# Kernel optimization log

Measured on AMD Instinct MI355X. Metric: run time of the kernel, lower is better.

Reference implementation:

```python
import jax, jax.numpy as jnp
import numpy as np

DIM = 512; NHEAD = 8; DHEAD = 64; INNER = NHEAD * DHEAD
CTX = 1024; NOCT = int(np.ceil(np.log2(CTX))) + 1  # 11
B = 8; SEQ = 256; MEM = 768


def positional_encoding(ctx, num_oct):
    # matches Attention.positional_encoding on coords=arange(ctx).view(ctx,1),
    # start_octave = 1 - num_oct
    coords = jnp.arange(ctx, dtype=jnp.float32)[:, None, None]        # (ctx,1,1)
    octaves = jnp.arange(1 - num_oct, 1, dtype=jnp.float32)           # (num_oct,)
    mult = (2.0 ** octaves) * np.pi
    scaled = (coords * mult).reshape(ctx, num_oct)                    # (ctx, num_oct)
    return jnp.concatenate([jnp.sin(scaled), jnp.cos(scaled)], axis=-1)  # (ctx, 2*num_oct)


def get_shifts(mem, seq, ctx):
    coords = jnp.arange(mem + seq - 1, -1, -1) - (seq - 1)            # (mem+seq,)
    shifts = coords[None, :] + jnp.arange(seq)[:, None]               # (seq, mem+seq)
    oob = (shifts < 0) | (shifts > ctx - 1)
    bias = jnp.where(oob, -jnp.inf, 0.0).astype(jnp.float32)
    return jnp.clip(shifts, 0, ctx - 1), bias


def setup_inputs() -> dict:
    key = jax.random.key(0)
    ks = jax.random.split(key, 8)
    s = 0.02
    return {
        "x": jax.random.normal(ks[0], (B, SEQ, DIM), jnp.float32),
        "memory": jax.random.normal(ks[1], (B, MEM, DIM), jnp.float32),
        "W_qkv": jax.random.normal(ks[2], (DIM, 3 * INNER), jnp.float32) * s,
        "W_rel": jax.random.normal(ks[3], (2 * NOCT, INNER), jnp.float32) * s,
        "W_out": jax.random.normal(ks[4], (INNER, DIM), jnp.float32) * s,
        "b_out": jnp.zeros((DIM,), jnp.float32),
        "u_emb": jax.random.normal(ks[5], (DHEAD,), jnp.float32),
        "v_emb": jax.random.normal(ks[6], (DHEAD,), jnp.float32),
    }


def reference(x, memory, W_qkv, W_rel, W_out, b_out, u_emb, v_emb):
    b, seq, _ = x.shape
    mem = memory.shape[1]
    total = mem + seq
    scale = DHEAD ** -0.5

    shifts, bias = get_shifts(mem, seq, CTX)                          # (seq,total) each
    R = positional_encoding(CTX, NOCT)                                # (CTX, 2*NOCT)
    kr = (R @ W_rel)[shifts].reshape(seq, total, NHEAD, DHEAD)        # n m h d

    qkv = jnp.concatenate([memory, x], axis=1) @ W_qkv                # (b,total,3*INNER)
    q, k, v = jnp.split(qkv, 3, axis=-1)

    def heads(t):
        return t.reshape(b, total, NHEAD, DHEAD).transpose(0, 2, 1, 3)  # b h m d

    q = heads(q)[:, :, mem:]                                          # b h n d (queries only over x)
    k = heads(k)
    v = heads(v)

    term_a = jnp.einsum('bhnd,bhmd->bhnm', q, k)
    term_b = jnp.einsum('bhnd,nmhd->bhnm', q, kr)
    term_c = jnp.einsum('d,bhmd->bhm', u_emb, k)[:, :, None, :]        # broadcast over n
    term_d = jnp.einsum('d,nmhd->hnm', v_emb, kr)[None]                # broadcast over b

    dots = (term_a + term_b + term_c + term_d) * scale + bias          # banded -inf mask
    attn = jax.nn.softmax(dots, axis=-1)                               # dropout p=0 -> identity
    out = jnp.einsum('bhnm,bhmd->bnhd', attn, v).reshape(b, seq, INNER)
    return out @ W_out + b_out
```

## Files before the change

kernel.cpp:

```cpp
#include <hip/hip_runtime.h>
#include <hip/hip_bf16.h>
#include <math.h>

typedef unsigned short u16;
typedef unsigned int u32;
typedef __attribute__((ext_vector_type(8))) short short8;
typedef __attribute__((ext_vector_type(4))) float floatx4;

constexpr int kB     = 8;
constexpr int kSEQ   = 256;
constexpr int kMEM   = 768;
constexpr int kTOTAL = 1024;

__device__ __forceinline__ float bf2f(u16 u) {
  return __uint_as_float(((u32)u) << 16);
}
__device__ __forceinline__ u16 f2bf(float f) {
  __hip_bfloat16 h = __float2bfloat16(f);
  return *reinterpret_cast<u16*>(&h);
}
__device__ __forceinline__ void gload_lds16(const u16* g, u16* l) {
  __builtin_amdgcn_global_load_lds(
      (__attribute__((address_space(1))) const unsigned int*)g,
      (__attribute__((address_space(3))) unsigned int*)l, 16, 0, 0);
}

__device__ __forceinline__ void wtconv_body(
    const float* __restrict__ W, u16* __restrict__ Wt, int K, int N,
    int n0, int k0, int tid, float (*tile)[65])
{
  int r = tid >> 4, c4 = (tid & 15) * 4;
#pragma unroll
  for (int v = 0; v < 4; v++) {
    float4 w4 = *(const float4*)(W + (size_t)(k0 + v * 16 + r) * N + n0 + c4);
    tile[v * 16 + r][c4 + 0] = w4.x;
    tile[v * 16 + r][c4 + 1] = w4.y;
    tile[v * 16 + r][c4 + 2] = w4.z;
    tile[v * 16 + r][c4 + 3] = w4.w;
  }
  __syncthreads();
#pragma unroll
  for (int v = 0; v < 4; v++) {
    int rn = v * 16 + r;
    ushort4 o;
    o.x = f2bf(tile[c4 + 0][rn]);
    o.y = f2bf(tile[c4 + 1][rn]);
    o.z = f2bf(tile[c4 + 2][rn]);
    o.w = f2bf(tile[c4 + 3][rn]);
    *(ushort4*)(Wt + (size_t)(n0 + rn) * K + k0 + c4) = o;
  }
}

__global__ __launch_bounds__(256) void prep_kernel(
    const float* __restrict__ x, const float* __restrict__ memf,
    const float* __restrict__ W_qkv, const float* __restrict__ W_out,
    const float* __restrict__ W_rel, const float* __restrict__ v_emb,
    u16* __restrict__ Xb, u16* __restrict__ WqkvT, u16* __restrict__ WoutT,
    u16* __restrict__ Rrel_bf, float* __restrict__ vR)
{
  __shared__ float tile[64][65];
  __shared__ float pe[22];
  __shared__ float prod[512];
  int bid = blockIdx.x;
  int t = threadIdx.x;
  if (bid < 1024) {
    int s = bid;
    if (t < 22) {
      int o = (t < 11) ? t : (t - 11);
      float mult = ldexpf(3.14159265358979323846f, o - 10);
      float ang = (float)s * mult;
      pe[t] = (t < 11) ? sinf(ang) : cosf(ang);
    }
    __syncthreads();
#pragma unroll
    for (int c = 0; c < 2; c++) {
      int j = t + c * 256;
      float acc = 0.f;
#pragma unroll
      for (int o = 0; o < 22; ++o) acc += pe[o] * W_rel[o * 512 + j];
      Rrel_bf[(size_t)s * 512 + j] = f2bf(acc);
      prod[j] = acc * v_emb[j & 63];
    }
    __syncthreads();
    if (t < 8) {
      float a = 0.f;
#pragma unroll 8
      for (int d = 0; d < 64; d++) a += prod[t * 64 + d];
      vR[t * 1024 + s] = a * 0.125f;
    }
  } else if (bid < 3072) {
    int idx = (bid - 1024) * 256 + t;
    int row = idx >> 6, c8 = idx & 63;
    int b = row >> 10, pos = row & 1023;
    const float* src = (pos < kMEM)
        ? memf + (size_t)(b * kMEM + pos) * 512
        : x    + (size_t)(b * kSEQ + pos - kMEM) * 512;
    const float4* s4 = (const float4*)(src + c8 * 8);
    float4 a = s4[0], bb = s4[1];
    u16 tmp[8] = {f2bf(a.x),  f2bf(a.y),  f2bf(a.z),  f2bf(a.w),
                  f2bf(bb.x), f2bf(bb.y), f2bf(bb.z), f2bf(bb.w)};
    *(uint4*)(Xb + (size_t)row * 512 + c8 * 8) = *(uint4*)tmp;
  } else if (bid < 3264) {
    int r = bid - 3072;
    wtconv_body(W_qkv, WqkvT, 512, 1536, (r % 24) * 64, (r / 24) * 64, t, tile);
  } else {
    int r = bid - 3264;
    wtconv_body(W_out, WoutT, 512, 512, (r % 8) * 64, (r / 8) * 64, t, tile);
  }
}

__global__ __launch_bounds__(256) void gemm_bf16(
    const u16* __restrict__ A, const u16* __restrict__ Bt,
    int lda, int ldb, int ksteps,
    u16* __restrict__ Cbf, int ldc, int qscale)
{
  __shared__ u16 As[128 * 64];
  __shared__ u16 Bs[128 * 64];
  int tid = threadIdx.x;
  int id = blockIdx.y * gridDim.x + blockIdx.x;
  int gy = gridDim.y;
  int bm = (id % gy) * 128, bn = (id / gy) * 128;
  int ln = tid & 15, quad = (tid >> 4) & 3, w = tid >> 6;
  int moff = (w >> 1) * 64, noff = (w & 1) * 64;
  int l7 = ln & 7;
  floatx4 acc[4][4];
#pragma unroll
  for (int mi = 0; mi < 4; mi++)
#pragma unroll
    for (int ni = 0; ni < 4; ni++) acc[mi][ni] = (floatx4){0.f, 0.f, 0.f, 0.f};

  int srow[4], sgch[4];
#pragma unroll
  for (int v = 0; v < 4; v++) {
    int f = v * 256 + tid;
    srow[v] = f >> 3;
    sgch[v] = (f & 7) ^ ((f >> 3) & 7);
  }

  for (int ks = 0; ks < ksteps; ks++) {
    int k0 = ks * 64;
#pragma unroll
    for (int v = 0; v < 4; v++) {
      gload_lds16(A + (size_t)(bm + srow[v]) * lda + k0 + sgch[v] * 8,
                  &As[(v * 256 + tid) * 8]);
      gload_lds16(Bt + (size_t)(bn + srow[v]) * ldb + k0 + sgch[v] * 8,
                  &Bs[(v * 256 + tid) * 8]);
    }
    __syncthreads();
#pragma unroll
    for (int kb = 0; kb < 2; kb++) {
      short8 af[4], bfr[4];
#pragma unroll
      for (int mi = 0; mi < 4; mi++) {
        int row = moff + mi * 16 + ln;
        af[mi] = *(const short8*)&As[row * 64 + (((quad + 4 * kb) ^ l7) << 3)];
      }
#pragma unroll
      for (int ni = 0; ni < 4; ni++) {
        int row = noff + ni * 16 + ln;
        bfr[ni] = *(const short8*)&Bs[row * 64 + (((quad + 4 * kb) ^ l7) << 3)];
      }
#pragma unroll
      for (int mi = 0; mi < 4; mi++)
#pragma unroll
        for (int ni = 0; ni < 4; ni++)
          acc[mi][ni] = __builtin_amdgcn_mfma_f32_16x16x32_bf16(
              af[mi], bfr[ni], acc[mi][ni], 0, 0, 0);
    }
    __syncthreads();
  }

  int r0 = bm + moff + quad * 4;
#pragma unroll
  for (int ni = 0; ni < 4; ni++) {
    int col = bn + noff + ni * 16 + ln;
    float scale = (qscale && col < 512) ? 0.125f : 1.f;
#pragma unroll
    for (int mi = 0; mi < 4; mi++) {
#pragma unroll
      for (int r = 0; r < 4; r++) {
        int row = r0 + mi * 16 + r;
        Cbf[(size_t)row * ldc + col] = f2bf(acc[mi][ni][r] * scale);
      }
    }
  }
}

__global__ __launch_bounds__(256) void gemm_bf16_64(
    const u16* __restrict__ A, const u16* __restrict__ Bt,
    int lda, int ldb, int ksteps,
    float* __restrict__ Cf, int ldc, const float* __restrict__ bias)
{
  __shared__ u16 As[64 * 64];
  __shared__ u16 Bs[64 * 64];
  int tid = threadIdx.x;
  int id = blockIdx.y * gridDim.x + blockIdx.x;
  int gy = gridDim.y;
  int bm = (id % gy) * 64, bn = (id / gy) * 64;
  int ln = tid & 15, quad = (tid >> 4) & 3, w = tid >> 6;
  int moff = (w >> 1) * 32, noff = (w & 1) * 32;
  int l7 = ln & 7;
  floatx4 acc[2][2];
#pragma unroll
  for (int mi = 0; mi < 2; mi++)
#pragma unroll
    for (int ni = 0; ni < 2; ni++) acc[mi][ni] = (floatx4){0.f, 0.f, 0.f, 0.f};

  int srow[2], sgch[2];
#pragma unroll
  for (int v = 0; v < 2; v++) {
    int f = v * 256 + tid;
    srow[v] = f >> 3;
    sgch[v] = (f & 7) ^ ((f >> 3) & 7);
  }

  for (int ks = 0; ks < ksteps; ks++) {
    int k0 = ks * 64;
#pragma unroll
    for (int v = 0; v < 2; v++) {
      gload_lds16(A + (size_t)(bm + srow[v]) * lda + k0 + sgch[v] * 8,
                  &As[(v * 256 + tid) * 8]);
      gload_lds16(Bt + (size_t)(bn + srow[v]) * ldb + k0 + sgch[v] * 8,
                  &Bs[(v * 256 + tid) * 8]);
    }
    __syncthreads();
#pragma unroll
    for (int kb = 0; kb < 2; kb++) {
      short8 af[2], bfr[2];
#pragma unroll
      for (int mi = 0; mi < 2; mi++) {
        int row = moff + mi * 16 + ln;
        af[mi] = *(const short8*)&As[row * 64 + (((quad + 4 * kb) ^ l7) << 3)];
      }
#pragma unroll
      for (int ni = 0; ni < 2; ni++) {
        int row = noff + ni * 16 + ln;
        bfr[ni] = *(const short8*)&Bs[row * 64 + (((quad + 4 * kb) ^ l7) << 3)];
      }
#pragma unroll
      for (int mi = 0; mi < 2; mi++)
#pragma unroll
        for (int ni = 0; ni < 2; ni++)
          acc[mi][ni] = __builtin_amdgcn_mfma_f32_16x16x32_bf16(
              af[mi], bfr[ni], acc[mi][ni], 0, 0, 0);
    }
    __syncthreads();
  }

  int r0 = bm + moff + quad * 4;
#pragma unroll
  for (int ni = 0; ni < 2; ni++) {
    int col = bn + noff + ni * 16 + ln;
    float cv = bias[col];
#pragma unroll
    for (int mi = 0; mi < 2; mi++) {
#pragma unroll
      for (int r = 0; r < 4; r++) {
        int row = r0 + mi * 16 + r;
        Cf[(size_t)row * ldc + col] = acc[mi][ni][r] + cv;
      }
    }
  }
}

__global__ __launch_bounds__(256) void attn_mfma(
    const u16* __restrict__ qkv_bf, const u16* __restrict__ Rrel_bf,
    const float* __restrict__ vR, const float* __restrict__ u_emb,
    u16* __restrict__ Opart, float* __restrict__ lbuf)
{
  constexpr int LD  = 72;
  constexpr int TLD = 84;
  __shared__ u16 Vt[2][64 * LD];
  __shared__ u16 Ps[64 * LD];
  __shared__ u16 Tl[4 * 16 * TLD];

  int nt = blockIdx.x >> 3, p = blockIdx.x & 7;
  int h = blockIdx.y, b = blockIdx.z;
  int n0 = nt * 64, bh = b * 8 + h;
  int tid = threadIdx.x;
  int w = tid >> 6, lane = tid & 63;
  int l15 = lane & 15, quad = lane >> 4, q8 = quad * 8;

  int sr0 = tid >> 3, sc8 = tid & 7;
  int sr1 = (256 + tid) >> 3;
  int vg0 = ((sr0 >> 3) ^ sc8) * 8 + (sr0 & 7);
  int vg1 = ((sr1 >> 3) ^ sc8) * 8 + (sr1 & 7);

  const u16* qrow = qkv_bf + (size_t)(b * kTOTAL + kMEM + n0 + 16 * w + l15) * 1536 + h * 64;
  short8 qf0 = *(const short8*)(qrow + q8);
  short8 qf1 = *(const short8*)(qrow + 32 + q8);

  short8 uf0, uf1;
  {
    u16 t0[8], t1[8];
#pragma unroll
    for (int j = 0; j < 8; j++) {
      t0[j] = f2bf(0.125f * u_emb[q8 + j]);
      t1[j] = f2bf(0.125f * u_emb[32 + q8 + j]);
    }
    uf0 = *(short8*)t0;
    uf1 = *(short8*)t1;
  }

  const u16* kpart = qkv_bf + (size_t)(b * kTOTAL) * 1536 + 512 + h * 64;
  const float* vRh = vR + h * 1024;
  u16* Tw = Tl + w * 16 * TLD;

  int ntiles = 13 + nt;
  int mtA = p, mtB = p + 8;
  bool hasB = (mtB < ntiles);
  bool lastB = (mtB == ntiles - 1);

  {
    const u16* va = kpart + (size_t)mtA * 64 * 1536 + 512;
    const u16* vb = kpart + (size_t)mtB * 64 * 1536 + 512;
    uint4 a0 = *(const uint4*)(va + (size_t)sr0 * 1536 + sc8 * 8);
    uint4 a1 = *(const uint4*)(va + (size_t)sr1 * 1536 + sc8 * 8);
    uint4 b0 = *(const uint4*)(vb + (size_t)sr0 * 1536 + sc8 * 8);
    uint4 b1 = *(const uint4*)(vb + (size_t)sr1 * 1536 + sc8 * 8);
    const u16* pa0v = (const u16*)&a0;
    const u16* pa1v = (const u16*)&a1;
    const u16* pb0v = (const u16*)&b0;
    const u16* pb1v = (const u16*)&b1;
#pragma unroll
    for (int i = 0; i < 8; i++) {
      Vt[0][(sc8 * 8 + i) * LD + vg0] = pa0v[i];
      Vt[0][(sc8 * 8 + i) * LD + vg1] = pa1v[i];
      Vt[1][(sc8 * 8 + i) * LD + vg0] = pb0v[i];
      Vt[1][(sc8 * 8 + i) * LD + vg1] = pb1v[i];
    }
  }
  __syncthreads();

  floatx4 o_acc[4];
  float l_i[4];
#pragma unroll
  for (int r = 0; r < 4; r++) l_i[r] = 0.f;
#pragma unroll
  for (int nd = 0; nd < 4; nd++) o_acc[nd] = (floatx4){0.f, 0.f, 0.f, 0.f};

  int s_base_w = kMEM + n0 + 16 * w;

  auto tile_body = [&](int mt, bool lastt, const u16* VtX) {
    int m0 = mt * 64;
    const u16* kbase = kpart + (size_t)m0 * 1536;
    int sb = s_base_w - m0;

    short8 kb0[4], kb1[4];
#pragma unroll
    for (int ni = 0; ni < 4; ni++) {
      const u16* kr = kbase + (size_t)(16 * ni + l15) * 1536;
      kb0[ni] = *(const short8*)(kr + q8);
      kb1[ni] = *(const short8*)(kr + 32 + q8);
    }
    short8 rb0[5], rb1[5];
    float vRc[5];
#pragma unroll
    for (int ct = 0; ct < 5; ct++) {
      int s = sb - 63 + 16 * ct + l15;
      s = min(max(s, 0), 1023);
      const u16* rr = Rrel_bf + (size_t)s * 512 + h * 64;
      rb0[ct] = *(const short8*)(rr + q8);
      rb1[ct] = *(const short8*)(rr + 32 + q8);
      vRc[ct] = vRh[s];
    }

    floatx4 uku[4];
#pragma unroll
    for (int ni = 0; ni < 4; ni++) {
      floatx4 ua = (floatx4){0.f, 0.f, 0.f, 0.f};
      ua = __builtin_amdgcn_mfma_f32_16x16x32_bf16(uf0, kb0[ni], ua, 0, 0, 0);
      ua = __builtin_amdgcn_mfma_f32_16x16x32_bf16(uf1, kb1[ni], ua, 0, 0, 0);
      uku[ni] = ua;
    }

#pragma unroll
    for (int ct = 0; ct < 5; ct++) {
      floatx4 t = (floatx4){0.f, 0.f, 0.f, 0.f};
      t = __builtin_amdgcn_mfma_f32_16x16x32_bf16(qf0, rb0[ct], t, 0, 0, 0);
      t = __builtin_amdgcn_mfma_f32_16x16x32_bf16(qf1, rb1[ct], t, 0, 0, 0);
#pragma unroll
      for (int r = 0; r < 4; r++)
        Tw[(4 * quad + r) * TLD + 16 * ct + l15] = f2bf(t[r] + vRc[ct]);
    }

    floatx4 s_acc[4];
#pragma unroll
    for (int ni = 0; ni < 4; ni++) {
      floatx4 sa = (floatx4){0.f, 0.f, 0.f, 0.f};
      sa = __builtin_amdgcn_mfma_f32_16x16x32_bf16(qf0, kb0[ni], sa, 0, 0, 0);
      sa = __builtin_amdgcn_mfma_f32_16x16x32_bf16(qf1, kb1[ni], sa, 0, 0, 0);
      s_acc[ni] = sa;
    }

#pragma unroll
    for (int r = 0; r < 4; r++) {
      int il = 4 * quad + r;
      float ls = 0.f;
      float pv[4];
#pragma unroll
      for (int ni = 0; ni < 4; ni++) {
        float tsh = bf2f(Tw[il * TLD + 63 + il - 16 * ni - l15]);
        float val = s_acc[ni][r] + tsh + uku[ni][r];
        if (lastt && (16 * ni + l15) > (16 * w + il)) val = -1e30f;
        float e = __expf(val);
        pv[ni] = e;
        ls += e;
      }
      l_i[r] += ls;
      int prow = 16 * w + il;
      int rr3p = prow >> 3;
      int base = prow * LD + (l15 & 7);
#pragma unroll
      for (int ni = 0; ni < 4; ni++)
        Ps[base + (((2 * ni + (l15 >> 3)) ^ rr3p) << 3)] = f2bf(pv[ni]);
    }

    int rowq = 16 * w + l15, rr3q = rowq >> 3;
    short8 pa0 = *(const short8*)&Ps[rowq * LD + ((quad ^ rr3q) << 3)];
    short8 pa1 = *(const short8*)&Ps[rowq * LD + (((quad + 4) ^ rr3q) << 3)];
#pragma unroll
    for (int nd = 0; nd < 4; nd++) {
      int rowv = 16 * nd + l15, rr3v = rowv >> 3;
      short8 vb0 = *(const short8*)&VtX[rowv * LD + ((quad ^ rr3v) << 3)];
      short8 vb1 = *(const short8*)&VtX[rowv * LD + (((quad + 4) ^ rr3v) << 3)];
      o_acc[nd] = __builtin_amdgcn_mfma_f32_16x16x32_bf16(pa0, vb0, o_acc[nd], 0, 0, 0);
      o_acc[nd] = __builtin_amdgcn_mfma_f32_16x16x32_bf16(pa1, vb1, o_acc[nd], 0, 0, 0);
    }
  };

  tile_body(mtA, false, Vt[0]);
  if (hasB) tile_body(mtB, lastB, Vt[1]);

  int pbase = (p * 64 + bh) * 256;
#pragma unroll
  for (int r = 0; r < 4; r++) {
    float l = l_i[r];
#pragma unroll
    for (int off = 1; off < 16; off <<= 1)
      l += __shfl_xor(l, off, 64);
    int n = n0 + 16 * w + 4 * quad + r;
    u16* orow = Opart + ((size_t)(pbase + n) << 6) + l15;
#pragma unroll
    for (int nd = 0; nd < 4; nd++)
      orow[16 * nd] = f2bf(o_acc[nd][r]);
    if (l15 == 0) lbuf[pbase + n] = l;
  }
}

__global__ __launch_bounds__(256) void attn_combine(
    const u16* __restrict__ Opart, const float* __restrict__ lbuf,
    u16* __restrict__ aout_bf)
{
  int idx = blockIdx.x * 256 + threadIdx.x;
  int bh = idx >> 12, n = (idx >> 4) & 255, d4 = idx & 15;
  int rowi = bh * 256 + n;
  float den = 0.f;
  float num[4] = {0.f, 0.f, 0.f, 0.f};
#pragma unroll
  for (int p = 0; p < 8; p++) {
    den += lbuf[(p << 14) + rowi];
    uint2 raw = *(const uint2*)(Opart + (((size_t)(p << 14) + rowi) << 6) + d4 * 4);
    const u16* us = (const u16*)&raw;
#pragma unroll
    for (int j = 0; j < 4; j++) num[j] += bf2f(us[j]);
  }
  float inv = 1.f / den;
  int b = bh >> 3, h = bh & 7;
  ushort4 o;
  o.x = f2bf(num[0] * inv);
  o.y = f2bf(num[1] * inv);
  o.z = f2bf(num[2] * inv);
  o.w = f2bf(num[3] * inv);
  *(ushort4*)(aout_bf + (size_t)(b * kSEQ + n) * 512 + h * 64 + d4 * 4) = o;
}

extern "C" void kernel_launch(void* const* d_in, const int* in_sizes, int n_in,
                              void* d_out, int out_size, void* d_ws, size_t ws_size,
                              hipStream_t stream) {
  (void)in_sizes; (void)n_in; (void)out_size; (void)ws_size;
  const float* x      = (const float*)d_in[0];
  const float* memory = (const float*)d_in[1];
  const float* W_qkv  = (const float*)d_in[2];
  const float* W_rel  = (const float*)d_in[3];
  const float* W_out  = (const float*)d_in[4];
  const float* b_out  = (const float*)d_in[5];
  const float* u_emb  = (const float*)d_in[6];
  const float* v_emb  = (const float*)d_in[7];
  float* out = (float*)d_out;

  char* ws = (char*)d_ws;
  u16*   qkv_bf  = (u16*)ws;                         ws += (size_t)12582912 * 2;
  u16*   Xcat_bf = (u16*)ws;                         ws += (size_t)4194304 * 2;
  u16*   aout_bf = (u16*)ws;                         ws += (size_t)1048576 * 2;
  u16*   Opart   = (u16*)ws;                         ws += (size_t)8388608 * 2;
  float* lbuf    = (float*)ws;                       ws += (size_t)131072 * 4;
  u16*   WqkvT   = (u16*)ws;                         ws += (size_t)786432 * 2;
  u16*   WoutT   = (u16*)ws;                         ws += (size_t)262144 * 2;
  u16*   Rrel_bf = (u16*)ws;                         ws += (size_t)524288 * 2;
  float* vR      = (float*)ws;                       ws += (size_t)8192 * 4;

  prep_kernel<<<3328, 256, 0, stream>>>(
      x, memory, W_qkv, W_out, W_rel, v_emb, Xcat_bf, WqkvT, WoutT, Rrel_bf, vR);

  gemm_bf16<<<dim3(12, 64), 256, 0, stream>>>(
      Xcat_bf, WqkvT, 512, 512, 8, qkv_bf, 1536, 1);

  attn_mfma<<<dim3(32, 8, 8), 256, 0, stream>>>(
      qkv_bf, Rrel_bf, vR, u_emb, Opart, lbuf);

  attn_combine<<<1024, 256, 0, stream>>>(Opart, lbuf, aout_bf);

  gemm_bf16_64<<<dim3(8, 32), 256, 0, stream>>>(
      aout_bf, WoutT, 512, 512, 8, out, 512, b_out);
}
```

Before: 158.7 us.

## Split attention into one key tile per block with variable-count combine

Each attention block now processes a single 64-key tile instead of two, doubling the grid and exiting early for tiles beyond the causal range. The combine kernel sums a per-row variable number of partials (13-16). This aims to raise occupancy and remove load imbalance from blocks with one or two tiles. In exchange it doubles the partial output buffer written and read, and gives up intra-block overlap across tiles.

Result: no change. 159.9 us (+0.8%).

```diff
diff --git a/kernel.cpp b/kernel.cpp
--- a/kernel.cpp
+++ b/kernel.cpp
@@ -270,11 +270,15 @@
 {
   constexpr int LD  = 72;
   constexpr int TLD = 84;
-  __shared__ u16 Vt[2][64 * LD];
+  __shared__ u16 Vt[64 * LD];
   __shared__ u16 Ps[64 * LD];
   __shared__ u16 Tl[4 * 16 * TLD];
 
-  int nt = blockIdx.x >> 3, p = blockIdx.x & 7;
+  int nt = blockIdx.x >> 4, p = blockIdx.x & 15;
+  int ntiles = 13 + nt;
+  if (p >= ntiles) return;
+  bool lastt = (p == ntiles - 1);
+
   int h = blockIdx.y, b = blockIdx.z;
   int n0 = nt * 64, bh = b * 8 + h;
   int tid = threadIdx.x;
@@ -286,6 +290,23 @@
   int vg0 = ((sr0 >> 3) ^ sc8) * 8 + (sr0 & 7);
   int vg1 = ((sr1 >> 3) ^ sc8) * 8 + (sr1 & 7);
 
+  const u16* kpart = qkv_bf + (size_t)(b * kTOTAL) * 1536 + 512 + h * 64;
+  int m0 = p * 64;
+  const u16* kbase = kpart + (size_t)m0 * 1536;
+
+  {
+    const u16* va = kbase + 512;
+    uint4 a0 = *(const uint4*)(va + (size_t)sr0 * 1536 + sc8 * 8);
+    uint4 a1 = *(const uint4*)(va + (size_t)sr1 * 1536 + sc8 * 8);
+    const u16* pa0v = (const u16*)&a0;
+    const u16* pa1v = (const u16*)&a1;
+#pragma unroll
+    for (int i = 0; i < 8; i++) {
+      Vt[(sc8 * 8 + i) * LD + vg0] = pa0v[i];
+      Vt[(sc8 * 8 + i) * LD + vg1] = pa1v[i];
+    }
+  }
+
   const u16* qrow = qkv_bf + (size_t)(b * kTOTAL + kMEM + n0 + 16 * w + l15) * 1536 + h * 64;
   short8 qf0 = *(const short8*)(qrow + q8);
   short8 qf1 = *(const short8*)(qrow + 32 + q8);
@@ -302,135 +323,98 @@
     uf1 = *(short8*)t1;
   }
 
-  const u16* kpart = qkv_bf + (size_t)(b * kTOTAL) * 1536 + 512 + h * 64;
   const float* vRh = vR + h * 1024;
   u16* Tw = Tl + w * 16 * TLD;
-
-  int ntiles = 13 + nt;
-  int mtA = p, mtB = p + 8;
-  bool hasB = (mtB < ntiles);
-  bool lastB = (mtB == ntiles - 1);
-
-  {
-    const u16* va = kpart + (size_t)mtA * 64 * 1536 + 512;
-    const u16* vb = kpart + (size_t)mtB * 64 * 1536 + 512;
-    uint4 a0 = *(const uint4*)(va + (size_t)sr0 * 1536 + sc8 * 8);
-    uint4 a1 = *(const uint4*)(va + (size_t)sr1 * 1536 + sc8 * 8);
-    uint4 b0 = *(const uint4*)(vb + (size_t)sr0 * 1536 + sc8 * 8);
-    uint4 b1 = *(const uint4*)(vb + (size_t)sr1 * 1536 + sc8 * 8);
-    const u16* pa0v = (const u16*)&a0;
-    const u16* pa1v = (const u16*)&a1;
-    const u16* pb0v = (const u16*)&b0;
-    const u16* pb1v = (const u16*)&b1;
-#pragma unroll
-    for (int i = 0; i < 8; i++) {
-      Vt[0][(sc8 * 8 + i) * LD + vg0] = pa0v[i];
-      Vt[0][(sc8 * 8 + i) * LD + vg1] = pa1v[i];
-      Vt[1][(sc8 * 8 + i) * LD + vg0] = pb0v[i];
-      Vt[1][(sc8 * 8 + i) * LD + vg1] = pb1v[i];
-    }
-  }
+  int s_base_w = kMEM + n0 + 16 * w;
+  int sb = s_base_w - m0;
+
+  short8 kb0[4], kb1[4];
+#pragma unroll
+  for (int ni = 0; ni < 4; ni++) {
+    const u16* kr = kbase + (size_t)(16 * ni + l15) * 1536;
+    kb0[ni] = *(const short8*)(kr + q8);
+    kb1[ni] = *(const short8*)(kr + 32 + q8);
+  }
+  short8 rb0[5], rb1[5];
+  float vRc[5];
+#pragma unroll
+  for (int ct = 0; ct < 5; ct++) {
+    int s = sb - 63 + 16 * ct + l15;
+    s = min(max(s, 0), 1023);
+    const u16* rr = Rrel_bf + (size_t)s * 512 + h * 64;
+    rb0[ct] = *(const short8*)(rr + q8);
+    rb1[ct] = *(const short8*)(rr + 32 + q8);
+    vRc[ct] = vRh[s];
+  }
+
   __syncthreads();
+
+  floatx4 uku[4];
+#pragma unroll
+  for (int ni = 0; ni < 4; ni++) {
+    floatx4 ua = (floatx4){0.f, 0.f, 0.f, 0.f};
+    ua = __builtin_amdgcn_mfma_f32_16x16x32_bf16(uf0, kb0[ni], ua, 0, 0, 0);
+    ua = __builtin_amdgcn_mfma_f32_16x16x32_bf16(uf1, kb1[ni], ua, 0, 0, 0);
+    uku[ni] = ua;
+  }
+
+#pragma unroll
+  for (int ct = 0; ct < 5; ct++) {
+    floatx4 t = (floatx4){0.f, 0.f, 0.f, 0.f};
+    t = __builtin_amdgcn_mfma_f32_16x16x32_bf16(qf0, rb0[ct], t, 0, 0, 0);
+    t = __builtin_amdgcn_mfma_f32_16x16x32_bf16(qf1, rb1[ct], t, 0, 0, 0);
+#pragma unroll
+    for (int r = 0; r < 4; r++)
+      Tw[(4 * quad + r) * TLD + 16 * ct + l15] = f2bf(t[r] + vRc[ct]);
+  }
+
+  floatx4 s_acc[4];
+#pragma unroll
+  for (int ni = 0; ni < 4; ni++) {
+    floatx4 sa = (floatx4){0.f, 0.f, 0.f, 0.f};
+    sa = __builtin_amdgcn_mfma_f32_16x16x32_bf16(qf0, kb0[ni], sa, 0, 0, 0);
+    sa = __builtin_amdgcn_mfma_f32_16x16x32_bf16(qf1, kb1[ni], sa, 0, 0, 0);
+    s_acc[ni] = sa;
+  }
 
   floatx4 o_acc[4];
   float l_i[4];
 #pragma unroll
-  for (int r = 0; r < 4; r++) l_i[r] = 0.f;
-#pragma unroll
   for (int nd = 0; nd < 4; nd++) o_acc[nd] = (floatx4){0.f, 0.f, 0.f, 0.f};
-
-  int s_base_w = kMEM + n0 + 16 * w;
-
-  auto tile_body = [&](int mt, bool lastt, const u16* VtX) {
-    int m0 = mt * 64;
-    const u16* kbase = kpart + (size_t)m0 * 1536;
-    int sb = s_base_w - m0;
-
-    short8 kb0[4], kb1[4];
+#pragma unroll
+  for (int r = 0; r < 4; r++) {
+    int il = 4 * quad + r;
+    float ls = 0.f;
+    float pv[4];
 #pragma unroll
     for (int ni = 0; ni < 4; ni++) {
-      const u16* kr = kbase + (size_t)(16 * ni + l15) * 1536;
-      kb0[ni] = *(const short8*)(kr + q8);
-      kb1[ni] = *(const short8*)(kr + 32 + q8);
-    }
-    short8 rb0[5], rb1[5];
-    float vRc[5];
-#pragma unroll
-    for (int ct = 0; ct < 5; ct++) {
-      int s = sb - 63 + 16 * ct + l15;
-      s = min(max(s, 0), 1023);
-      const u16* rr = Rrel_bf + (size_t)s * 512 + h * 64;
-      rb0[ct] = *(const short8*)(rr + q8);
-      rb1[ct] = *(const short8*)(rr + 32 + q8);
-      vRc[ct] = vRh[s];
-    }
-
-    floatx4 uku[4];
-#pragma unroll
-    for (int ni = 0; ni < 4; ni++) {
-      floatx4 ua = (floatx4){0.f, 0.f, 0.f, 0.f};
-      ua = __builtin_amdgcn_mfma_f32_16x16x32_bf16(uf0, kb0[ni], ua, 0, 0, 0);
-      ua = __builtin_amdgcn_mfma_f32_16x16x32_bf16(uf1, kb1[ni], ua, 0, 0, 0);
-      uku[ni] = ua;
-    }
-
-#pragma unroll
-    for (int ct = 0; ct < 5; ct++) {
-      floatx4 t = (floatx4){0.f, 0.f, 0.f, 0.f};
-      t = __builtin_amdgcn_mfma_f32_16x16x32_bf16(qf0, rb0[ct], t, 0, 0, 0);
-      t = __builtin_amdgcn_mfma_f32_16x16x32_bf16(qf1, rb1[ct], t, 0, 0, 0);
-#pragma unroll
-      for (int r = 0; r < 4; r++)
-        Tw[(4 * quad + r) * TLD + 16 * ct + l15] = f2bf(t[r] + vRc[ct]);
-    }
-
-    floatx4 s_acc[4];
-#pragma unroll
-    for (int ni = 0; ni < 4; ni++) {
-      floatx4 sa = (floatx4){0.f, 0.f, 0.f, 0.f};
-      sa = __builtin_amdgcn_mfma_f32_16x16x32_bf16(qf0, kb0[ni], sa, 0, 0, 0);
-      sa = __builtin_amdgcn_mfma_f32_16x16x32_bf16(qf1, kb1[ni], sa, 0, 0, 0);
-      s_acc[ni] = sa;
-    }
-
-#pragma unroll
-    for (int r = 0; r < 4; r++) {
-      int il = 4 * quad + r;
-      float ls = 0.f;
-      float pv[4];
-#pragma unroll
-      for (int ni = 0; ni < 4; ni++) {
-        float tsh = bf2f(Tw[il * TLD + 63 + il - 16 * ni - l15]);
-        float val = s_acc[ni][r] + tsh + uku[ni][r];
-        if (lastt && (16 * ni + l15) > (16 * w + il)) val = -1e30f;
-        float e = __expf(val);
-        pv[ni] = e;
-        ls += e;
-      }
-      l_i[r] += ls;
-      int prow = 16 * w + il;
-      int rr3p = prow >> 3;
-      int base = prow * LD + (l15 & 7);
-#pragma unroll
-      for (int ni = 0; ni < 4; ni++)
-        Ps[base + (((2 * ni + (l15 >> 3)) ^ rr3p) << 3)] = f2bf(pv[ni]);
-    }
-
-    int rowq = 16 * w + l15, rr3q = rowq >> 3;
-    short8 pa0 = *(const short8*)&Ps[rowq * LD + ((quad ^ rr3q) << 3)];
-    short8 pa1 = *(const short8*)&Ps[rowq * LD + (((quad + 4) ^ rr3q) << 3)];
-#pragma unroll
-    for (int nd = 0; nd < 4; nd++) {
-      int rowv = 16 * nd + l15, rr3v = rowv >> 3;
-      short8 vb0 = *(const short8*)&VtX[rowv * LD + ((quad ^ rr3v) << 3)];
-      short8 vb1 = *(const short8*)&VtX[rowv * LD + (((quad + 4) ^ rr3v) << 3)];
-      o_acc[nd] = __builtin_amdgcn_mfma_f32_16x16x32_bf16(pa0, vb0, o_acc[nd], 0, 0, 0);
-      o_acc[nd] = __builtin_amdgcn_mfma_f32_16x16x32_bf16(pa1, vb1, o_acc[nd], 0, 0, 0);
-    }
-  };
-
-  tile_body(mtA, false, Vt[0]);
-  if (hasB) tile_body(mtB, lastB, Vt[1]);
+      float tsh = bf2f(Tw[il * TLD + 63 + il - 16 * ni - l15]);
+      float val = s_acc[ni][r] + tsh + uku[ni][r];
+      if (lastt && (16 * ni + l15) > (16 * w + il)) val = -1e30f;
+      float e = __expf(val);
+      pv[ni] = e;
+      ls += e;
+    }
+    l_i[r] = ls;
+    int prow = 16 * w + il;
+    int rr3p = prow >> 3;
+    int base = prow * LD + (l15 & 7);
+#pragma unroll
+    for (int ni = 0; ni < 4; ni++)
+      Ps[base + (((2 * ni + (l15 >> 3)) ^ rr3p) << 3)] = f2bf(pv[ni]);
+  }
+
+  int rowq = 16 * w + l15, rr3q = rowq >> 3;
+  short8 pa0 = *(const short8*)&Ps[rowq * LD + ((quad ^ rr3q) << 3)];
+  short8 pa1 = *(const short8*)&Ps[rowq * LD + (((quad + 4) ^ rr3q) << 3)];
+#pragma unroll
+  for (int nd = 0; nd < 4; nd++) {
+    int rowv = 16 * nd + l15, rr3v = rowv >> 3;
+    short8 vb0 = *(const short8*)&Vt[rowv * LD + ((quad ^ rr3v) << 3)];
+    short8 vb1 = *(const short8*)&Vt[rowv * LD + (((quad + 4) ^ rr3v) << 3)];
+    o_acc[nd] = __builtin_amdgcn_mfma_f32_16x16x32_bf16(pa0, vb0, o_acc[nd], 0, 0, 0);
+    o_acc[nd] = __builtin_amdgcn_mfma_f32_16x16x32_bf16(pa1, vb1, o_acc[nd], 0, 0, 0);
+  }
 
   int pbase = (p * 64 + bh) * 256;
 #pragma unroll
@@ -455,10 +439,10 @@
   int idx = blockIdx.x * 256 + threadIdx.x;
   int bh = idx >> 12, n = (idx >> 4) & 255, d4 = idx & 15;
   int rowi = bh * 256 + n;
+  int plim = 13 + (n >> 6);
   float den = 0.f;
   float num[4] = {0.f, 0.f, 0.f, 0.f};
-#pragma unroll
-  for (int p = 0; p < 8; p++) {
+  for (int p = 0; p < plim; p++) {
     den += lbuf[(p << 14) + rowi];
     uint2 raw = *(const uint2*)(Opart + (((size_t)(p << 14) + rowi) << 6) + d4 * 4);
     const u16* us = (const u16*)&raw;
@@ -493,8 +477,8 @@
   u16*   qkv_bf  = (u16*)ws;                         ws += (size_t)12582912 * 2;
   u16*   Xcat_bf = (u16*)ws;                         ws += (size_t)4194304 * 2;
   u16*   aout_bf = (u16*)ws;                         ws += (size_t)1048576 * 2;
-  u16*   Opart   = (u16*)ws;                         ws += (size_t)8388608 * 2;
-  float* lbuf    = (float*)ws;                       ws += (size_t)131072 * 4;
+  u16*   Opart   = (u16*)ws;                         ws += (size_t)16777216 * 2;
+  float* lbuf    = (float*)ws;                       ws += (size_t)262144 * 4;
   u16*   WqkvT   = (u16*)ws;                         ws += (size_t)786432 * 2;
   u16*   WoutT   = (u16*)ws;                         ws += (size_t)262144 * 2;
   u16*   Rrel_bf = (u16*)ws;                         ws += (size_t)524288 * 2;
@@ -506,7 +490,7 @@
   gemm_bf16<<<dim3(12, 64), 256, 0, stream>>>(
       Xcat_bf, WqkvT, 512, 512, 8, qkv_bf, 1536, 1);
 
-  attn_mfma<<<dim3(32, 8, 8), 256, 0, stream>>>(
+  attn_mfma<<<dim3(64, 8, 8), 256, 0, stream>>>(
       qkv_bf, Rrel_bf, vR, u_emb, Opart, lbuf);
 
   attn_combine<<<1024, 256, 0, stream>>>(Opart, lbuf, aout_bf);
```
